# Kernel tuning notes

Measured on AMD Instinct MI355X. Metric: run time of the kernel, lower is better.

## Reference

```python
import jax, jax.numpy as jnp
import numpy as np

NUM_HEADS = 16


def setup_inputs() -> dict:
    key = jax.random.key(0)
    ks = jax.random.split(key, 8)
    B_, N, C = 2048, 64, 512
    nW = 64
    return {
        "x": jax.random.normal(ks[0], (B_, N, C), dtype=jnp.float32),
        "pe": jax.random.normal(ks[1], (1, N, C), dtype=jnp.float32),
        "rpe": jax.random.normal(ks[2], (NUM_HEADS, N, N), dtype=jnp.float32),
        "mask": jax.random.normal(ks[3], (nW, N, N), dtype=jnp.float32),
        "qkv_w": jax.random.normal(ks[4], (3 * C, C), dtype=jnp.float32) * 0.02,
        "qkv_b": jax.random.normal(ks[5], (3 * C,), dtype=jnp.float32) * 0.02,
        "proj_w": jax.random.normal(ks[6], (C, C), dtype=jnp.float32) * 0.02,
        "proj_b": jax.random.normal(ks[7], (C,), dtype=jnp.float32) * 0.02,
    }


def reference(x, pe, rpe, mask, qkv_w, qkv_b, proj_w, proj_b):
    B_, N, C = x.shape
    H = NUM_HEADS
    hd = C // H
    scale = hd ** -0.5
    xp = x + pe  # (B_, N, C)
    qkv = xp @ qkv_w.T + qkv_b  # (B_, N, 3C)
    qkv = qkv.reshape(B_, N, 3, H, hd).transpose(2, 0, 3, 1, 4)  # (3, B_, H, N, hd)
    q, k, v = qkv[0], qkv[1], qkv[2]
    attn = jnp.einsum("bhnd,bhmd->bhnm", q * scale, k)  # (B_, H, N, N)
    attn = attn + rpe[None]  # broadcast rpe over batch
    nW = mask.shape[0]
    attn = attn.reshape(B_ // nW, nW, H, N, N) + mask[None, :, None]
    attn = attn.reshape(B_, H, N, N)
    attn = jax.nn.softmax(attn, axis=-1)
    out = jnp.einsum("bhnm,bhmd->bhnd", attn, v)  # (B_, H, N, hd)
    out = out.transpose(0, 2, 1, 3).reshape(B_, N, C)
    return out @ proj_w.T + proj_b
```

## Files before the change

### kernel.cpp

```cpp
#include <hip/hip_runtime.h>
#include <hip/hip_bf16.h>
#include <cstdint>

typedef __bf16 bf16;
typedef __bf16 bf16x8_t __attribute__((ext_vector_type(8)));
typedef __bf16 bf16x4_t __attribute__((ext_vector_type(4)));
typedef float  f32x4_t  __attribute__((ext_vector_type(4)));

#define MFMA16(a, b, c) __builtin_amdgcn_mfma_f32_16x16x32_bf16((a), (b), (c), 0, 0, 0)

__global__ void k_wprep(const float* __restrict__ wq, const float* __restrict__ wp,
                        bf16* __restrict__ wqb, bf16* __restrict__ wpb) {
    int t = blockIdx.x * 256 + threadIdx.x;
    int stride = gridDim.x * 256;
    for (int i = t; i < 196608; i += stride) {
        float4 v = ((const float4*)wq)[i];
        bf16x4_t o; o[0]=(bf16)v.x; o[1]=(bf16)v.y; o[2]=(bf16)v.z; o[3]=(bf16)v.w;
        ((bf16x4_t*)wqb)[i] = o;
    }
    for (int i = t; i < 65536; i += stride) {
        float4 v = ((const float4*)wp)[i];
        bf16x4_t o; o[0]=(bf16)v.x; o[1]=(bf16)v.y; o[2]=(bf16)v.z; o[3]=(bf16)v.w;
        ((bf16x4_t*)wpb)[i] = o;
    }
}

__global__ __launch_bounds__(256, 2) void k_qkv(
    const float* __restrict__ x,
    const float* __restrict__ pe,
    const bf16*  __restrict__ Bw,
    const float* __restrict__ bias,
    bf16* __restrict__ Cq)
{
    __shared__ bf16 As[2][128 * 72];
    __shared__ bf16 Bs[2][128 * 72];

    const int tid  = threadIdx.x;
    const int lane = tid & 63;
    const int wave = tid >> 6;
    const int lr = lane & 15, lg = lane >> 4;
    const int wr = wave >> 1, wc = wave & 1;
    const int bid = blockIdx.x;
    const int wg  = (bid & 7) * 768 + (bid >> 3);
    const int mb  = wg / 12, nb = wg - mb * 12;
    const size_t m0 = (size_t)mb * 128;
    const int n0 = nb * 128;

    const int row = tid >> 3;
    const int i8  = (tid & 7) * 8;

    f32x4_t acc[4][4] = {};
    bf16x8_t va[4], vb[4];

    auto load_ab = [&](int kt) {
        const int k0 = kt * 64;
#pragma unroll
        for (int j = 0; j < 4; ++j) {
            int r = row + 32 * j;
            const float* xr = x  + (m0 + r) * 512 + k0 + i8;
            const float* pr = pe + (size_t)(r & 63) * 512 + k0 + i8;
            float4 x0 = *(const float4*)(xr);
            float4 x1 = *(const float4*)(xr + 4);
            float4 p0 = *(const float4*)(pr);
            float4 p1 = *(const float4*)(pr + 4);
            bf16x8_t v;
            v[0]=(bf16)(x0.x+p0.x); v[1]=(bf16)(x0.y+p0.y);
            v[2]=(bf16)(x0.z+p0.z); v[3]=(bf16)(x0.w+p0.w);
            v[4]=(bf16)(x1.x+p1.x); v[5]=(bf16)(x1.y+p1.y);
            v[6]=(bf16)(x1.z+p1.z); v[7]=(bf16)(x1.w+p1.w);
            va[j] = v;
            vb[j] = *(const bf16x8_t*)(Bw + (size_t)(n0 + r) * 512 + k0 + i8);
        }
    };
    auto write_lds = [&](int buf) {
#pragma unroll
        for (int j = 0; j < 4; ++j) {
            int r = row + 32 * j;
            *(bf16x8_t*)&As[buf][r * 72 + i8] = va[j];
            *(bf16x8_t*)&Bs[buf][r * 72 + i8] = vb[j];
        }
    };

    load_ab(0);
    write_lds(0);
    __syncthreads();

    for (int kt = 0; kt < 8; ++kt) {
        if (kt < 7) load_ab(kt + 1);
        const int cur = kt & 1;
#pragma unroll
        for (int k2 = 0; k2 < 2; ++k2) {
            bf16x8_t af[4], bfr[4];
#pragma unroll
            for (int i = 0; i < 4; ++i)
                af[i] = *(const bf16x8_t*)&As[cur][(wr * 64 + i * 16 + lr) * 72 + k2 * 32 + lg * 8];
#pragma unroll
            for (int j = 0; j < 4; ++j)
                bfr[j] = *(const bf16x8_t*)&Bs[cur][(wc * 64 + j * 16 + lr) * 72 + k2 * 32 + lg * 8];
#pragma unroll
            for (int i = 0; i < 4; ++i)
#pragma unroll
                for (int j = 0; j < 4; ++j)
                    acc[i][j] = MFMA16(af[i], bfr[j], acc[i][j]);
        }
        if (kt < 7) {
            write_lds(cur ^ 1);
            __syncthreads();
        }
    }

    float bj[4];
#pragma unroll
    for (int j = 0; j < 4; ++j) bj[j] = bias[n0 + wc * 64 + j * 16 + lr];
#pragma unroll
    for (int i = 0; i < 4; ++i)
#pragma unroll
        for (int j = 0; j < 4; ++j) {
            int col = n0 + wc * 64 + j * 16 + lr;
#pragma unroll
            for (int r = 0; r < 4; ++r) {
                size_t rw = m0 + wr * 64 + i * 16 + lg * 4 + r;
                Cq[rw * 1536 + col] = (bf16)(acc[i][j][r] + bj[j]);
            }
        }
}

__global__ __launch_bounds__(256, 2) void k_attn(
    const bf16*  __restrict__ qkv,
    const float* __restrict__ rpe,
    const float* __restrict__ mask,
    bf16* __restrict__ ao,
    int winbase)
{
    __shared__ bf16 vts[4][32 * 72];
    __shared__ bf16 ps[4][64 * 72];

    const int tid  = threadIdx.x;
    const int lane = tid & 63;
    const int wave = tid >> 6;
    const int lr   = lane & 15;
    const int lg   = lane >> 4;
    const int bw   = blockIdx.x;
    const int gw   = winbase + bw;
    const int wi   = gw & 63;
    const size_t qbase = (size_t)bw * 64 * 1536;
    const float* mp = mask + (size_t)wi * 4096;
    bf16* pvt = &vts[wave][0];
    bf16* pps = &ps[wave][0];

    const float SCALE = 0.17677669529663687f;

    for (int hh = 0; hh < 4; ++hh) {
        const int h  = wave * 4 + hh;
        const int hc = h * 32;
        const float* rp = rpe + (size_t)h * 4096;

        bf16x8_t qf[4], kf[4];
#pragma unroll
        for (int t = 0; t < 4; ++t) {
            qf[t] = *(const bf16x8_t*)(qkv + qbase + (size_t)(t * 16 + lr) * 1536 + hc + lg * 8);
            kf[t] = *(const bf16x8_t*)(qkv + qbase + (size_t)(t * 16 + lr) * 1536 + 512 + hc + lg * 8);
        }
#pragma unroll
        for (int j = 0; j < 4; ++j) {
            bf16x8_t vr = *(const bf16x8_t*)(qkv + qbase +
                (size_t)(j * 16 + (lane >> 2)) * 1536 + 1024 + hc + (lane & 3) * 8);
#pragma unroll
            for (int i = 0; i < 8; ++i)
                pvt[((lane & 3) * 8 + i) * 72 + j * 16 + (lane >> 2)] = vr[i];
        }

        float sminv[4][4];
#pragma unroll
        for (int mt = 0; mt < 4; ++mt) {
            f32x4_t s[4];
            f32x4_t zero = {};
#pragma unroll
            for (int nt = 0; nt < 4; ++nt)
                s[nt] = MFMA16(qf[mt], kf[nt], zero);
            float rm[4][4];
#pragma unroll
            for (int nt = 0; nt < 4; ++nt) {
                int col = nt * 16 + lr;
#pragma unroll
                for (int r = 0; r < 4; ++r) {
                    int rrow = mt * 16 + lg * 4 + r;
                    rm[nt][r] = rp[rrow * 64 + col] + mp[rrow * 64 + col];
                }
            }
            float mx[4] = {-1e30f, -1e30f, -1e30f, -1e30f};
#pragma unroll
            for (int nt = 0; nt < 4; ++nt)
#pragma unroll
                for (int r = 0; r < 4; ++r) {
                    float tv = s[nt][r] * SCALE + rm[nt][r];
                    s[nt][r] = tv;
                    mx[r] = fmaxf(mx[r], tv);
                }
#pragma unroll
            for (int r = 0; r < 4; ++r) {
                float m = mx[r];
                m = fmaxf(m, __shfl_xor(m, 1));
                m = fmaxf(m, __shfl_xor(m, 2));
                m = fmaxf(m, __shfl_xor(m, 4));
                m = fmaxf(m, __shfl_xor(m, 8));
                mx[r] = m;
            }
            float sm[4] = {0.f, 0.f, 0.f, 0.f};
#pragma unroll
            for (int nt = 0; nt < 4; ++nt)
#pragma unroll
                for (int r = 0; r < 4; ++r) {
                    float e = __expf(s[nt][r] - mx[r]);
                    s[nt][r] = e;
                    sm[r] += e;
                }
#pragma unroll
            for (int r = 0; r < 4; ++r) {
                float ssum = sm[r];
                ssum += __shfl_xor(ssum, 1);
                ssum += __shfl_xor(ssum, 2);
                ssum += __shfl_xor(ssum, 4);
                ssum += __shfl_xor(ssum, 8);
                sminv[mt][r] = 1.0f / ssum;
            }
#pragma unroll
            for (int nt = 0; nt < 4; ++nt)
#pragma unroll
                for (int r = 0; r < 4; ++r)
                    pps[(mt * 16 + lg * 4 + r) * 72 + nt * 16 + lr] = (bf16)s[nt][r];
        }

#pragma unroll
        for (int mt = 0; mt < 4; ++mt) {
            f32x4_t o[2] = {};
#pragma unroll
            for (int ks = 0; ks < 2; ++ks) {
                bf16x8_t pa = *(const bf16x8_t*)&pps[(mt * 16 + lr) * 72 + ks * 32 + lg * 8];
#pragma unroll
                for (int jd = 0; jd < 2; ++jd) {
                    bf16x8_t bv = *(const bf16x8_t*)&pvt[(jd * 16 + lr) * 72 + ks * 32 + lg * 8];
                    o[jd] = MFMA16(pa, bv, o[jd]);
                }
            }
#pragma unroll
            for (int jd = 0; jd < 2; ++jd)
#pragma unroll
                for (int r = 0; r < 4; ++r) {
                    size_t rrow = (size_t)gw * 64 + mt * 16 + lg * 4 + r;
                    ao[rrow * 512 + hc + jd * 16 + lr] = (bf16)(o[jd][r] * sminv[mt][r]);
                }
        }
    }
}

__global__ __launch_bounds__(256, 2) void k_proj(
    const bf16* __restrict__ A, const bf16* __restrict__ Bw,
    const float* __restrict__ bias, float* __restrict__ C)
{
    __shared__ bf16 As[2][128 * 72];
    __shared__ bf16 Bs[2][128 * 72];

    const int tid  = threadIdx.x;
    const int lane = tid & 63;
    const int wave = tid >> 6;
    const int lr = lane & 15, lg = lane >> 4;
    const int wr = wave >> 1, wc = wave & 1;
    const int bid = blockIdx.x;
    const int wg  = (bid & 7) * 512 + (bid >> 3);
    const int mb = wg >> 2, nb = wg & 3;
    const size_t m0 = (size_t)mb * 128;
    const int n0 = nb * 128;

    const int row = tid >> 3;
    const int i8  = (tid & 7) * 8;

    f32x4_t acc[4][4] = {};
    bf16x8_t va[4], vb[4];

    auto load_ab = [&](int kt) {
        const int k0 = kt * 64;
#pragma unroll
        for (int j = 0; j < 4; ++j) {
            int r = row + 32 * j;
            va[j] = *(const bf16x8_t*)(A  + (m0 + r) * 512 + k0 + i8);
            vb[j] = *(const bf16x8_t*)(Bw + (size_t)(n0 + r) * 512 + k0 + i8);
        }
    };
    auto write_lds = [&](int buf) {
#pragma unroll
        for (int j = 0; j < 4; ++j) {
            int r = row + 32 * j;
            *(bf16x8_t*)&As[buf][r * 72 + i8] = va[j];
            *(bf16x8_t*)&Bs[buf][r * 72 + i8] = vb[j];
        }
    };

    load_ab(0);
    write_lds(0);
    __syncthreads();

    for (int kt = 0; kt < 8; ++kt) {
        if (kt < 7) load_ab(kt + 1);
        const int cur = kt & 1;
#pragma unroll
        for (int k2 = 0; k2 < 2; ++k2) {
            bf16x8_t af[4], bfr[4];
#pragma unroll
            for (int i = 0; i < 4; ++i)
                af[i] = *(const bf16x8_t*)&As[cur][(wr * 64 + i * 16 + lr) * 72 + k2 * 32 + lg * 8];
#pragma unroll
            for (int j = 0; j < 4; ++j)
                bfr[j] = *(const bf16x8_t*)&Bs[cur][(wc * 64 + j * 16 + lr) * 72 + k2 * 32 + lg * 8];
#pragma unroll
            for (int i = 0; i < 4; ++i)
#pragma unroll
                for (int j = 0; j < 4; ++j)
                    acc[i][j] = MFMA16(af[i], bfr[j], acc[i][j]);
        }
        if (kt < 7) {
            write_lds(cur ^ 1);
            __syncthreads();
        }
    }

    float bj[4];
#pragma unroll
    for (int j = 0; j < 4; ++j) bj[j] = bias[n0 + wc * 64 + j * 16 + lr];
#pragma unroll
    for (int i = 0; i < 4; ++i)
#pragma unroll
        for (int j = 0; j < 4; ++j) {
            int col = n0 + wc * 64 + j * 16 + lr;
#pragma unroll
            for (int r = 0; r < 4; ++r) {
                size_t rw = m0 + wr * 64 + i * 16 + lg * 4 + r;
                C[rw * 512 + col] = acc[i][j][r] + bj[j];
            }
        }
}

extern "C" void kernel_launch(void* const* d_in, const int* in_sizes, int n_in,
                              void* d_out, int out_size, void* d_ws, size_t ws_size,
                              hipStream_t stream) {
    (void)in_sizes; (void)n_in; (void)out_size; (void)ws_size;
    const float* x      = (const float*)d_in[0];
    const float* pe     = (const float*)d_in[1];
    const float* rpe    = (const float*)d_in[2];
    const float* mask   = (const float*)d_in[3];
    const float* qkv_w  = (const float*)d_in[4];
    const float* qkv_b  = (const float*)d_in[5];
    const float* proj_w = (const float*)d_in[6];
    const float* proj_b = (const float*)d_in[7];
    float* out = (float*)d_out;

    char* ws = (char*)d_ws;
    bf16* wqkvb  = (bf16*)ws;
    bf16* wprojb = (bf16*)(ws + 1572864);
    bf16* ao     = (bf16*)(ws + 2097152);
    bf16* qkvscr = (bf16*)d_out;

    k_wprep<<<256, 256, 0, stream>>>(qkv_w, proj_w, wqkvb, wprojb);
    for (int pass = 0; pass < 2; ++pass) {
        k_qkv<<<6144, 256, 0, stream>>>(x + (size_t)pass * 65536 * 512, pe,
                                        wqkvb, qkv_b, qkvscr);
        k_attn<<<1024, 256, 0, stream>>>(qkvscr, rpe, mask, ao, pass * 1024);
    }
    k_proj<<<4096, 256, 0, stream>>>(ao, wprojb, proj_b, out);
}
```

Before: 839.9 us.

## Precompute bf16 x+pe, use direct global-to-LDS loads with XOR swizzle, head-major QKV layout

Adds a prepass that adds the positional embedding to x and converts it to bf16 once, so the QKV GEMM stops rereading fp32 x and pe for every N tile. Both GEMMs now stage tiles with global_load_lds straight into an XOR-swizzled LDS layout and use explicit waitcnt/barriers, avoiding the register round trip and the padding. The QKV output is written head-major per window so attention reads contiguous q/k/v. The work is split into four chunks instead of two. The cost is an extra pass over x writing 128MB of bf16 into the output buffer, plus a more fragile hand-managed synchronization scheme.

```diff
diff --git a/kernel.cpp b/kernel.cpp
--- a/kernel.cpp
+++ b/kernel.cpp
@@ -8,6 +8,13 @@
 typedef float  f32x4_t  __attribute__((ext_vector_type(4)));
 
 #define MFMA16(a, b, c) __builtin_amdgcn_mfma_f32_16x16x32_bf16((a), (b), (c), 0, 0, 0)
+
+__device__ __forceinline__ void gload_lds16(const bf16* g, bf16* l) {
+    __builtin_amdgcn_global_load_lds(
+        (const __attribute__((address_space(1))) void*)g,
+        (__attribute__((address_space(3))) void*)l,
+        16, 0, 0);
+}
 
 __global__ void k_wprep(const float* __restrict__ wq, const float* __restrict__ wp,
                         bf16* __restrict__ wqb, bf16* __restrict__ wpb) {
@@ -25,15 +32,36 @@
     }
 }
 
+__global__ void k_xprep(const float* __restrict__ x, const float* __restrict__ pe,
+                        bf16* __restrict__ xp) {
+    int t = blockIdx.x * 256 + threadIdx.x;
+    int stride = gridDim.x * 256;
+    for (int i = t; i < 8388608; i += stride) {
+        int row = i >> 6;
+        int g   = (i & 63) * 8;
+        const float* xr = x  + ((size_t)row << 9) + g;
+        const float* pr = pe + ((size_t)(row & 63) << 9) + g;
+        float4 x0 = *(const float4*)(xr);
+        float4 x1 = *(const float4*)(xr + 4);
+        float4 p0 = *(const float4*)(pr);
+        float4 p1 = *(const float4*)(pr + 4);
+        bf16x8_t v;
+        v[0]=(bf16)(x0.x+p0.x); v[1]=(bf16)(x0.y+p0.y);
+        v[2]=(bf16)(x0.z+p0.z); v[3]=(bf16)(x0.w+p0.w);
+        v[4]=(bf16)(x1.x+p1.x); v[5]=(bf16)(x1.y+p1.y);
+        v[6]=(bf16)(x1.z+p1.z); v[7]=(bf16)(x1.w+p1.w);
+        *(bf16x8_t*)(xp + (size_t)i * 8) = v;
+    }
+}
+
 __global__ __launch_bounds__(256, 2) void k_qkv(
-    const float* __restrict__ x,
-    const float* __restrict__ pe,
+    const bf16*  __restrict__ A,
     const bf16*  __restrict__ Bw,
     const float* __restrict__ bias,
     bf16* __restrict__ Cq)
 {
-    __shared__ bf16 As[2][128 * 72];
-    __shared__ bf16 Bs[2][128 * 72];
+    __shared__ bf16 As[2][128 * 64];
+    __shared__ bf16 Bs[2][128 * 64];
 
     const int tid  = threadIdx.x;
     const int lane = tid & 63;
@@ -41,71 +69,66 @@
     const int lr = lane & 15, lg = lane >> 4;
     const int wr = wave >> 1, wc = wave & 1;
     const int bid = blockIdx.x;
-    const int wg  = (bid & 7) * 768 + (bid >> 3);
+    const int wg  = (bid & 7) * 384 + (bid >> 3);
     const int mb  = wg / 12, nb = wg - mb * 12;
     const size_t m0 = (size_t)mb * 128;
     const int n0 = nb * 128;
 
-    const int row = tid >> 3;
-    const int i8  = (tid & 7) * 8;
-
     f32x4_t acc[4][4] = {};
-    bf16x8_t va[4], vb[4];
-
-    auto load_ab = [&](int kt) {
+
+    auto stage = [&](int kt, int buf) {
         const int k0 = kt * 64;
 #pragma unroll
-        for (int j = 0; j < 4; ++j) {
-            int r = row + 32 * j;
-            const float* xr = x  + (m0 + r) * 512 + k0 + i8;
-            const float* pr = pe + (size_t)(r & 63) * 512 + k0 + i8;
-            float4 x0 = *(const float4*)(xr);
-            float4 x1 = *(const float4*)(xr + 4);
-            float4 p0 = *(const float4*)(pr);
-            float4 p1 = *(const float4*)(pr + 4);
-            bf16x8_t v;
-            v[0]=(bf16)(x0.x+p0.x); v[1]=(bf16)(x0.y+p0.y);
-            v[2]=(bf16)(x0.z+p0.z); v[3]=(bf16)(x0.w+p0.w);
-            v[4]=(bf16)(x1.x+p1.x); v[5]=(bf16)(x1.y+p1.y);
-            v[6]=(bf16)(x1.z+p1.z); v[7]=(bf16)(x1.w+p1.w);
-            va[j] = v;
-            vb[j] = *(const bf16x8_t*)(Bw + (size_t)(n0 + r) * 512 + k0 + i8);
+        for (int ii = 0; ii < 4; ++ii) {
+            int instr = wave * 4 + ii;
+            int r  = instr * 8 + (lane >> 3);
+            int gp = (lane & 7) ^ (r & 7);
+            gload_lds16(A  + (m0 + r) * 512 + k0 + gp * 8, &As[buf][instr * 512]);
+            gload_lds16(Bw + (size_t)(n0 + r) * 512 + k0 + gp * 8, &Bs[buf][instr * 512]);
         }
     };
-    auto write_lds = [&](int buf) {
-#pragma unroll
-        for (int j = 0; j < 4; ++j) {
-            int r = row + 32 * j;
-            *(bf16x8_t*)&As[buf][r * 72 + i8] = va[j];
-            *(bf16x8_t*)&Bs[buf][r * 72 + i8] = vb[j];
-        }
-    };
-
-    load_ab(0);
-    write_lds(0);
-    __syncthreads();
+
+    stage(0, 0);
 
     for (int kt = 0; kt < 8; ++kt) {
-        if (kt < 7) load_ab(kt + 1);
         const int cur = kt & 1;
+        if (kt < 7) {
+            stage(kt + 1, cur ^ 1);
+            asm volatile("s_waitcnt vmcnt(8) lgkmcnt(0)" ::: "memory");
+        } else {
+            asm volatile("s_waitcnt vmcnt(0) lgkmcnt(0)" ::: "memory");
+        }
+        __builtin_amdgcn_sched_barrier(0);
+        __builtin_amdgcn_s_barrier();
+        __builtin_amdgcn_sched_barrier(0);
+
 #pragma unroll
         for (int k2 = 0; k2 < 2; ++k2) {
             bf16x8_t af[4], bfr[4];
 #pragma unroll
-            for (int i = 0; i < 4; ++i)
-                af[i] = *(const bf16x8_t*)&As[cur][(wr * 64 + i * 16 + lr) * 72 + k2 * 32 + lg * 8];
-#pragma unroll
-            for (int j = 0; j < 4; ++j)
-                bfr[j] = *(const bf16x8_t*)&Bs[cur][(wc * 64 + j * 16 + lr) * 72 + k2 * 32 + lg * 8];
+            for (int i = 0; i < 4; ++i) {
+                int rowa = wr * 64 + i * 16 + lr;
+                int ph   = (k2 * 4 + lg) ^ (rowa & 7);
+                af[i] = *(const bf16x8_t*)&As[cur][rowa * 64 + ph * 8];
+            }
+#pragma unroll
+            for (int j = 0; j < 4; ++j) {
+                int rowb = wc * 64 + j * 16 + lr;
+                int ph   = (k2 * 4 + lg) ^ (rowb & 7);
+                bfr[j] = *(const bf16x8_t*)&Bs[cur][rowb * 64 + ph * 8];
+            }
 #pragma unroll
             for (int i = 0; i < 4; ++i)
 #pragma unroll
                 for (int j = 0; j < 4; ++j)
                     acc[i][j] = MFMA16(af[i], bfr[j], acc[i][j]);
         }
+
         if (kt < 7) {
-            write_lds(cur ^ 1);
-            __syncthreads();
+            asm volatile("s_waitcnt lgkmcnt(0)" ::: "memory");
+            __builtin_amdgcn_sched_barrier(0);
+            __builtin_amdgcn_s_barrier();
+            __builtin_amdgcn_sched_barrier(0);
         }
     }
 
@@ -116,11 +139,16 @@
     for (int i = 0; i < 4; ++i)
 #pragma unroll
         for (int j = 0; j < 4; ++j) {
-            int col = n0 + wc * 64 + j * 16 + lr;
+            int col   = n0 + wc * 64 + j * 16 + lr;
+            int which = col >> 9;
+            int h     = (col >> 5) & 15;
+            int d     = col & 31;
+            bf16* base = Cq + (size_t)(which * 16 + h) * (512 * 2048);
 #pragma unroll
             for (int r = 0; r < 4; ++r) {
-                size_t rw = m0 + wr * 64 + i * 16 + lg * 4 + r;
-                Cq[rw * 1536 + col] = (bf16)(acc[i][j][r] + bj[j]);
+                int mrow = (int)m0 + wr * 64 + i * 16 + lg * 4 + r;
+                int win = mrow >> 6, tok = mrow & 63;
+                base[(size_t)win * 2048 + tok * 32 + d] = (bf16)(acc[i][j][r] + bj[j]);
             }
         }
 }
@@ -143,7 +171,6 @@
     const int bw   = blockIdx.x;
     const int gw   = winbase + bw;
     const int wi   = gw & 63;
-    const size_t qbase = (size_t)bw * 64 * 1536;
     const float* mp = mask + (size_t)wi * 4096;
     bf16* pvt = &vts[wave][0];
     bf16* pps = &ps[wave][0];
@@ -152,19 +179,20 @@
 
     for (int hh = 0; hh < 4; ++hh) {
         const int h  = wave * 4 + hh;
-        const int hc = h * 32;
         const float* rp = rpe + (size_t)h * 4096;
+        const bf16* qb = qkv + ((size_t)(h)      * 512 + bw) * 2048;
+        const bf16* kb = qkv + ((size_t)(16 + h) * 512 + bw) * 2048;
+        const bf16* vb = qkv + ((size_t)(32 + h) * 512 + bw) * 2048;
 
         bf16x8_t qf[4], kf[4];
 #pragma unroll
         for (int t = 0; t < 4; ++t) {
-            qf[t] = *(const bf16x8_t*)(qkv + qbase + (size_t)(t * 16 + lr) * 1536 + hc + lg * 8);
-            kf[t] = *(const bf16x8_t*)(qkv + qbase + (size_t)(t * 16 + lr) * 1536 + 512 + hc + lg * 8);
+            qf[t] = *(const bf16x8_t*)(qb + (t * 16 + lr) * 32 + lg * 8);
+            kf[t] = *(const bf16x8_t*)(kb + (t * 16 + lr) * 32 + lg * 8);
         }
 #pragma unroll
         for (int j = 0; j < 4; ++j) {
-            bf16x8_t vr = *(const bf16x8_t*)(qkv + qbase +
-                (size_t)(j * 16 + (lane >> 2)) * 1536 + 1024 + hc + (lane & 3) * 8);
+            bf16x8_t vr = *(const bf16x8_t*)(vb + (j * 16 + (lane >> 2)) * 32 + (lane & 3) * 8);
 #pragma unroll
             for (int i = 0; i < 8; ++i)
                 pvt[((lane & 3) * 8 + i) * 72 + j * 16 + (lane >> 2)] = vr[i];
@@ -248,7 +276,7 @@
 #pragma unroll
                 for (int r = 0; r < 4; ++r) {
                     size_t rrow = (size_t)gw * 64 + mt * 16 + lg * 4 + r;
-                    ao[rrow * 512 + hc + jd * 16 + lr] = (bf16)(o[jd][r] * sminv[mt][r]);
+                    ao[rrow * 512 + h * 32 + jd * 16 + lr] = (bf16)(o[jd][r] * sminv[mt][r]);
                 }
         }
     }
@@ -258,8 +286,8 @@
     const bf16* __restrict__ A, const bf16* __restrict__ Bw,
     const float* __restrict__ bias, float* __restrict__ C)
 {
-    __shared__ bf16 As[2][128 * 72];
-    __shared__ bf16 Bs[2][128 * 72];
+    __shared__ bf16 As[2][128 * 64];
+    __shared__ bf16 Bs[2][128 * 64];
 
     const int tid  = threadIdx.x;
     const int lane = tid & 63;
@@ -272,55 +300,61 @@
     const size_t m0 = (size_t)mb * 128;
     const int n0 = nb * 128;
 
-    const int row = tid >> 3;
-    const int i8  = (tid & 7) * 8;
-
     f32x4_t acc[4][4] = {};
-    bf16x8_t va[4], vb[4];
-
-    auto load_ab = [&](int kt) {
+
+    auto stage = [&](int kt, int buf) {
         const int k0 = kt * 64;
 #pragma unroll
-        for (int j = 0; j < 4; ++j) {
-            int r = row + 32 * j;
-            va[j] = *(const bf16x8_t*)(A  + (m0 + r) * 512 + k0 + i8);
-            vb[j] = *(const bf16x8_t*)(Bw + (size_t)(n0 + r) * 512 + k0 + i8);
+        for (int ii = 0; ii < 4; ++ii) {
+            int instr = wave * 4 + ii;
+            int r  = instr * 8 + (lane >> 3);
+            int gp = (lane & 7) ^ (r & 7);
+            gload_lds16(A  + (m0 + r) * 512 + k0 + gp * 8, &As[buf][instr * 512]);
+            gload_lds16(Bw + (size_t)(n0 + r) * 512 + k0 + gp * 8, &Bs[buf][instr * 512]);
         }
     };
-    auto write_lds = [&](int buf) {
-#pragma unroll
-        for (int j = 0; j < 4; ++j) {
-            int r = row + 32 * j;
-            *(bf16x8_t*)&As[buf][r * 72 + i8] = va[j];
-            *(bf16x8_t*)&Bs[buf][r * 72 + i8] = vb[j];
-        }
-    };
-
-    load_ab(0);
-    write_lds(0);
-    __syncthreads();
+
+    stage(0, 0);
 
     for (int kt = 0; kt < 8; ++kt) {
-        if (kt < 7) load_ab(kt + 1);
         const int cur = kt & 1;
+        if (kt < 7) {
+            stage(kt + 1, cur ^ 1);
+            asm volatile("s_waitcnt vmcnt(8) lgkmcnt(0)" ::: "memory");
+        } else {
+            asm volatile("s_waitcnt vmcnt(0) lgkmcnt(0)" ::: "memory");
+        }
+        __builtin_amdgcn_sched_barrier(0);
+        __builtin_amdgcn_s_barrier();
+        __builtin_amdgcn_sched_barrier(0);
+
 #pragma unroll
         for (int k2 = 0; k2 < 2; ++k2) {
             bf16x8_t af[4], bfr[4];
 #pragma unroll
-            for (int i = 0; i < 4; ++i)
-                af[i] = *(const bf16x8_t*)&As[cur][(wr * 64 + i * 16 + lr) * 72 + k2 * 32 + lg * 8];
-#pragma unroll
-            for (int j = 0; j < 4; ++j)
-                bfr[j] = *(const bf16x8_t*)&Bs[cur][(wc * 64 + j * 16 + lr) * 72 + k2 * 32 + lg * 8];
+            for (int i = 0; i < 4; ++i) {
+                int rowa = wr * 64 + i * 16 + lr;
+                int ph   = (k2 * 4 + lg) ^ (rowa & 7);
+                af[i] = *(const bf16x8_t*)&As[cur][rowa * 64 + ph * 8];
+            }
+#pragma unroll
+            for (int j = 0; j < 4; ++j) {
+                int rowb = wc * 64 + j * 16 + lr;
+                int ph   = (k2 * 4 + lg) ^ (rowb & 7);
+                bfr[j] = *(const bf16x8_t*)&Bs[cur][rowb * 64 + ph * 8];
+            }
 #pragma unroll
             for (int i = 0; i < 4; ++i)
 #pragma unroll
                 for (int j = 0; j < 4; ++j)
                     acc[i][j] = MFMA16(af[i], bfr[j], acc[i][j]);
         }
+
         if (kt < 7) {
-            write_lds(cur ^ 1);
-            __syncthreads();
+            asm volatile("s_waitcnt lgkmcnt(0)" ::: "memory");
+            __builtin_amdgcn_sched_barrier(0);
+            __builtin_amdgcn_s_barrier();
+            __builtin_amdgcn_sched_barrier(0);
         }
     }
 
@@ -358,13 +392,16 @@
     bf16* wqkvb  = (bf16*)ws;
     bf16* wprojb = (bf16*)(ws + 1572864);
     bf16* ao     = (bf16*)(ws + 2097152);
-    bf16* qkvscr = (bf16*)d_out;
+
+    bf16* xp   = (bf16*)d_out;
+    bf16* qkvc = (bf16*)((char*)d_out + 134217728);
 
     k_wprep<<<256, 256, 0, stream>>>(qkv_w, proj_w, wqkvb, wprojb);
-    for (int pass = 0; pass < 2; ++pass) {
-        k_qkv<<<6144, 256, 0, stream>>>(x + (size_t)pass * 65536 * 512, pe,
-                                        wqkvb, qkv_b, qkvscr);
-        k_attn<<<1024, 256, 0, stream>>>(qkvscr, rpe, mask, ao, pass * 1024);
+    k_xprep<<<4096, 256, 0, stream>>>(x, pe, xp);
+    for (int c = 0; c < 4; ++c) {
+        k_qkv<<<3072, 256, 0, stream>>>(xp + (size_t)c * 32768 * 512,
+                                        wqkvb, qkv_b, qkvc);
+        k_attn<<<512, 256, 0, stream>>>(qkvc, rpe, mask, ao, c * 512);
     }
     k_proj<<<4096, 256, 0, stream>>>(ao, wprojb, proj_b, out);
 }
```

Result: faster. 784.9 us (-6.6%).
